# Kernel tuning notes

Hardware: AMD Instinct MI355X
Metric: run time of the kernel (lower is better)

Reference implementation:

```python
import jax, jax.numpy as jnp
import numpy as np

# dims
N, Lx, Ff = 2048, 168, 64          # batch, encoder seq len, encoder features
HID = 256                           # GRU hidden size
Ly, Ft, FOUT, BINS = 72, 22, 10, 8  # decoder steps, future feats, output size, rain classes
DEC_IN = Ft + FOUT                  # 32, GRUCell input = cat(y_t, p)
REG_H, CLS_H = 128, 128             # head hidden widths
BETA = 1.1                          # SmeLU beta


def smelu(x):
    # SmeLU: 0 for x<=-b, x for x>=b, (x+b)^2/(4b) in between
    return jnp.where(x >= BETA, x,
                     jnp.where(x <= -BETA, jnp.zeros_like(x),
                               (x + BETA) ** 2 / (4.0 * BETA)))


def gru_step(h, u, Wih, Whh, bih, bhh):
    # torch GRU/GRUCell gate math; Wih: (3H, in), Whh: (3H, H)
    gi = u @ Wih.T + bih
    gh = h @ Whh.T + bhh
    i_r, i_z, i_n = jnp.split(gi, 3, axis=-1)
    h_r, h_z, h_n = jnp.split(gh, 3, axis=-1)
    r = jax.nn.sigmoid(i_r + h_r)
    z = jax.nn.sigmoid(i_z + h_z)
    n = jnp.tanh(i_n + r * h_n)
    return (1.0 - z) * n + z * h


def setup_inputs() -> dict:
    key = jax.random.key(0)
    ks = jax.random.split(key, 24)
    s = 1.0 / np.sqrt(HID)

    def rn(k, shape, scale):
        return jax.random.normal(k, shape, dtype=jnp.float32) * scale

    return {
        'x_f': rn(ks[0], (N, Lx, Ff), 1.0),
        'x': rn(ks[1], (N, Lx, FOUT), 1.0),      # unused by forward (matches torch)
        'y_t': rn(ks[2], (N, Ly + 1, Ft), 1.0),
        'p': rn(ks[3], (N, Ly + 1, FOUT), 1.0),
        # encoder GRU (1 layer, unidirectional)
        'enc_Wih': rn(ks[4], (3 * HID, Ff), s), 'enc_Whh': rn(ks[5], (3 * HID, HID), s),
        'enc_bih': rn(ks[6], (3 * HID,), s), 'enc_bhh': rn(ks[7], (3 * HID,), s),
        # decoder GRUCell
        'dec_Wih': rn(ks[8], (3 * HID, DEC_IN), s), 'dec_Whh': rn(ks[9], (3 * HID, HID), s),
        'dec_bih': rn(ks[10], (3 * HID,), s), 'dec_bhh': rn(ks[11], (3 * HID,), s),
        # temphr head: HID -> REG_H -> (FOUT - BINS)
        'th_W0': rn(ks[12], (REG_H, HID), s), 'th_b0': rn(ks[13], (REG_H,), s),
        'th_W1': rn(ks[14], (FOUT - BINS, REG_H), 1.0 / np.sqrt(REG_H)), 'th_b1': rn(ks[15], (FOUT - BINS,), 0.05),
        # class head: HID -> CLS_H -> BINS
        'cl_W0': rn(ks[16], (CLS_H, HID), s), 'cl_b0': rn(ks[17], (CLS_H,), s),
        'cl_W1': rn(ks[18], (BINS, CLS_H), 1.0 / np.sqrt(CLS_H)), 'cl_b1': rn(ks[19], (BINS,), 0.05),
    }


def reference(x_f, x, y_t, p,
              enc_Wih, enc_Whh, enc_bih, enc_bhh,
              dec_Wih, dec_Whh, dec_bih, dec_bhh,
              th_W0, th_b0, th_W1, th_b1,
              cl_W0, cl_b0, cl_W1, cl_b1):
    # ---- encoder: run GRU over Lx, keep final hidden (N, HID) ----
    h0 = jnp.zeros((x_f.shape[0], HID), dtype=x_f.dtype)
    enc_xs = jnp.swapaxes(x_f, 0, 1)  # (Lx, N, Ff)

    def enc_body(h, u):
        return gru_step(h, u, enc_Wih, enc_Whh, enc_bih, enc_bhh), None

    h_enc, _ = jax.lax.scan(enc_body, h0, enc_xs)

    # ---- decoder inputs: torch loop uses cat(y_t,p) at index 0, then i-1 ----
    ytp = jnp.concatenate([y_t[:, :-1, :], p[:, :-1, :]], axis=-1)  # (N, Ly, DEC_IN)
    idx = jnp.concatenate([jnp.zeros((1,), jnp.int32), jnp.arange(Ly - 1, dtype=jnp.int32)])
    dec_in = jnp.swapaxes(ytp[:, idx, :], 0, 1)  # (Ly, N, DEC_IN)

    def dec_body(h, u):
        h2 = gru_step(h, u, dec_Wih, dec_Whh, dec_bih, dec_bhh)
        th = smelu(h2 @ th_W0.T + th_b0) @ th_W1.T + th_b1   # (N, 2)
        cl = smelu(h2 @ cl_W0.T + cl_b0) @ cl_W1.T + cl_b1   # (N, BINS)
        return h2, jnp.concatenate([th, cl], axis=-1)

    _, outs = jax.lax.scan(dec_body, h_enc, dec_in)  # (Ly, N, FOUT)
    return jnp.swapaxes(outs, 0, 1)  # (N, Ly, FOUT)
```

## Files before the change

### kernel.cpp

```cpp
#include <hip/hip_runtime.h>

typedef __bf16 v8bf __attribute__((ext_vector_type(8)));
typedef float v4f __attribute__((ext_vector_type(4)));
typedef float v4ff __attribute__((ext_vector_type(4)));
typedef unsigned short u16;
typedef unsigned int u32;

#define DEVI __device__ __forceinline__

constexpr int LX = 168, FF = 64;
constexpr int LY = 72, FT = 22, FOUTC = 10;
constexpr int HID = 256;
constexpr int HSTR = 264;
constexpr int UST2 = 40;
constexpr int SSTR = 264;

constexpr int W_EWIH = 0;
constexpr int W_EWHH = 49152;
constexpr int W_DWIH = 245760;
constexpr int W_DWHH = 270336;
constexpr int W_THW0 = 466944;
constexpr int W_THW1 = 499712;
constexpr int W_CLW0 = 499968;
constexpr int W_CLW1 = 532736;
constexpr int W_TOTAL = 533760;

DEVI u16 f2bf(float f) {
  u32 x; __builtin_memcpy(&x, &f, 4);
  return (u16)((x + 0x7FFFu + ((x >> 16) & 1u)) >> 16);
}
DEVI float sigm(float x) { return __builtin_amdgcn_rcpf(1.f + __expf(-x)); }
DEVI float tanh_(float x) {
  float e = __expf(-2.f * fabsf(x));
  return copysignf((1.f - e) * __builtin_amdgcn_rcpf(1.f + e), x);
}
DEVI float smelu_(float x) {
  if (x >= 1.1f) return x;
  if (x <= -1.1f) return 0.f;
  float u = x + 1.1f;
  return u * u * (1.f / 4.4f);
}
DEVI v8bf ld8(const u16* p) { return *reinterpret_cast<const v8bf*>(p); }
DEVI v4f ldw(const u16* p) { return *reinterpret_cast<const v4f*>(p); }
DEVI v8bf asbf(v4f x) { return __builtin_bit_cast(v8bf, x); }
DEVI void pin(v4f& x) { asm("" : "+v"(x)); }
DEVI v4f mfma16(v8bf a, v8bf b, v4f c) {
  return __builtin_amdgcn_mfma_f32_16x16x32_bf16(a, b, c, 0, 0, 0);
}
DEVI v8bf cvt2f(v4ff lo, v4ff hi) {
  v8bf r;
#pragma unroll
  for (int j = 0; j < 4; ++j) { r[j] = (__bf16)lo[j]; r[4 + j] = (__bf16)hi[j]; }
  return r;
}

__global__ void cvt_weights(const float* __restrict__ eWih, const float* __restrict__ eWhh,
                            const float* __restrict__ dWih, const float* __restrict__ dWhh,
                            const float* __restrict__ thW0, const float* __restrict__ thW1,
                            const float* __restrict__ clW0, const float* __restrict__ clW1,
                            u16* __restrict__ ws) {
  const int i = blockIdx.x * 256 + threadIdx.x;
  if (i >= W_TOTAL) return;
  const float* src; int off;
  if      (i < W_EWHH) { src = eWih; off = W_EWIH; }
  else if (i < W_DWIH) { src = eWhh; off = W_EWHH; }
  else if (i < W_DWHH) { src = dWih; off = W_DWIH; }
  else if (i < W_THW0) { src = dWhh; off = W_DWHH; }
  else if (i < W_THW1) { src = thW0; off = W_THW0; }
  else if (i < W_CLW0) { src = thW1; off = W_THW1; }
  else if (i < W_CLW1) { src = clW0; off = W_CLW0; }
  else                 { src = clW1; off = W_CLW1; }
  ws[i] = f2bf(src[i - off]);
}

__global__ __launch_bounds__(512, 2) void encdec_kernel(
    const float* __restrict__ xf, const float* __restrict__ yt, const float* __restrict__ pp,
    const float* __restrict__ ebih, const float* __restrict__ ebhh,
    const float* __restrict__ dbih, const float* __restrict__ dbhh,
    const float* __restrict__ thb0, const float* __restrict__ thb1,
    const float* __restrict__ clb0, const float* __restrict__ clb1,
    const u16* __restrict__ ws, float* __restrict__ outp) {
  __shared__ __align__(16) u16 slab[256 * SSTR];
  __shared__ __align__(16) u16 hls[2][16 * HSTR];
  __shared__ __align__(16) u16 a1x[16 * HSTR];
  __shared__ __align__(16) u16 uls[2][16 * UST2];

  const u16* eWih = ws + W_EWIH;
  const u16* eWhh = ws + W_EWHH;
  const u16* dWih = ws + W_DWIH;
  const u16* dWhh = ws + W_DWHH;
  const u16* thW0 = ws + W_THW0;
  const u16* thW1 = ws + W_THW1;
  const u16* clW0 = ws + W_CLW0;
  const u16* clW1 = ws + W_CLW1;

  const int tid = threadIdx.x;
  const int wave = tid >> 6;
  const int lane = tid & 63;
  const int col16 = lane & 15;
  const int quad = lane >> 4;
  const int n0 = blockIdx.x * 16;

  for (int i = tid; i < 16 * HSTR; i += 512) hls[0][i] = 0;

  float hreg[2][4];
#pragma unroll
  for (int j = 0; j < 2; ++j)
#pragma unroll
    for (int r = 0; r < 4; ++r) hreg[j][r] = 0.f;

  v4f wz[2][8], wn[2][8];
  float bsr[2], bsz[2], bin_[2], bhn[2];

  {
    for (int i = tid; i < 256 * 32; i += 512) {
      const int row = i >> 5, kb = (i & 31) << 3;
      *reinterpret_cast<v8bf*>(&slab[row * SSTR + kb]) = ld8(eWhh + row * HID + kb);
    }
#pragma unroll
    for (int j = 0; j < 2; ++j) {
      const int c = wave + 8 * j;
      const int mr = c * 16 + col16, mz = 256 + mr, mn = 512 + mr;
#pragma unroll
      for (int k = 0; k < 8; ++k) {
        wz[j][k] = ldw(eWhh + (size_t)mz * HID + k * 32 + quad * 8); pin(wz[j][k]);
        wn[j][k] = ldw(eWhh + (size_t)mn * HID + k * 32 + quad * 8); pin(wn[j][k]);
      }
      bsr[j] = ebih[mr] + ebhh[mr];
      bsz[j] = ebih[mz] + ebhh[mz];
      bin_[j] = ebih[mn];
      bhn[j] = ebhh[mn];
    }
    const float* xbase = xf + (size_t)(n0 + col16) * LX * FF + quad * 8;
    const u16* sp0 = slab + (wave * 16 + col16) * SSTR + quad * 8;
    const u16* sp1 = slab + ((wave + 8) * 16 + col16) * SSTR + quad * 8;
    __syncthreads();

#pragma unroll 1
    for (int t = 0; t < LX; ++t) {
      const float* xr = xbase + (size_t)t * FF;
      const v4ff x0 = *(const v4ff*)(xr);
      const v4ff x1 = *(const v4ff*)(xr + 4);
      const v4ff x2 = *(const v4ff*)(xr + 32);
      const v4ff x3 = *(const v4ff*)(xr + 36);
      const u16* hb = hls[t & 1] + col16 * HSTR + quad * 8;
      v8bf a[8];
#pragma unroll
      for (int k = 0; k < 8; ++k) a[k] = ld8(hb + k * 32);

      v4f az[2] = {{0.f,0.f,0.f,0.f},{0.f,0.f,0.f,0.f}};
      v4f ar[2] = {{0.f,0.f,0.f,0.f},{0.f,0.f,0.f,0.f}};
      v4f an[2] = {{0.f,0.f,0.f,0.f},{0.f,0.f,0.f,0.f}};
#pragma unroll
      for (int k = 0; k < 8; ++k) {
        az[0] = mfma16(a[k], asbf(wz[0][k]), az[0]);
        az[1] = mfma16(a[k], asbf(wz[1][k]), az[1]);
        ar[0] = mfma16(a[k], ld8(sp0 + k * 32), ar[0]);
        ar[1] = mfma16(a[k], ld8(sp1 + k * 32), ar[1]);
        an[0] = mfma16(a[k], asbf(wn[0][k]), an[0]);
        an[1] = mfma16(a[k], asbf(wn[1][k]), an[1]);
      }
      const v8bf xa0 = cvt2f(x0, x1);
      const v8bf xa1 = cvt2f(x2, x3);
      v4f ai[2] = {{0.f,0.f,0.f,0.f},{0.f,0.f,0.f,0.f}};
#pragma unroll
      for (int j = 0; j < 2; ++j) {
        const int m = (wave + 8 * j) * 16 + col16;
        const u16* pwr = eWih + (size_t)m * FF + quad * 8;
        const u16* pwz = eWih + (size_t)(256 + m) * FF + quad * 8;
        const u16* pwn = eWih + (size_t)(512 + m) * FF + quad * 8;
        az[j] = mfma16(xa0, ld8(pwz), az[j]);
        az[j] = mfma16(xa1, ld8(pwz + 32), az[j]);
        ar[j] = mfma16(xa0, ld8(pwr), ar[j]);
        ar[j] = mfma16(xa1, ld8(pwr + 32), ar[j]);
        ai[j] = mfma16(xa0, ld8(pwn), ai[j]);
        ai[j] = mfma16(xa1, ld8(pwn + 32), ai[j]);
      }
#pragma unroll
      for (int j = 0; j < 2; ++j) {
        const int cidx = (wave + 8 * j) * 16 + col16;
#pragma unroll
        for (int r = 0; r < 4; ++r) {
          const float zg = sigm(az[j][r] + bsz[j]);
          const float rg = sigm(ar[j][r] + bsr[j]);
          const float ng = tanh_(ai[j][r] + bin_[j] + rg * (an[j][r] + bhn[j]));
          hreg[j][r] = (1.f - zg) * ng + zg * hreg[j][r];
          hls[(t + 1) & 1][(quad * 4 + r) * HSTR + cidx] = f2bf(hreg[j][r]);
        }
      }
      __syncthreads();
    }
  }

  {
    for (int i = tid; i < 256 * 32; i += 512) {
      const int row = i >> 5, kb = (i & 31) << 3;
      *reinterpret_cast<v8bf*>(&slab[row * SSTR + kb]) = ld8(dWhh + row * HID + kb);
    }
    float hb0[2];
#pragma unroll
    for (int j = 0; j < 2; ++j) {
      const int c = wave + 8 * j;
      const int mr = c * 16 + col16, mz = 256 + mr, mn = 512 + mr;
#pragma unroll
      for (int k = 0; k < 8; ++k) {
        wz[j][k] = ldw(dWhh + (size_t)mz * HID + k * 32 + quad * 8); pin(wz[j][k]);
        wn[j][k] = ldw(dWhh + (size_t)mn * HID + k * 32 + quad * 8); pin(wn[j][k]);
      }
      bsr[j] = dbih[mr] + dbhh[mr];
      bsz[j] = dbih[mz] + dbhh[mz];
      bin_[j] = dbih[mn];
      bhn[j] = dbhh[mn];
      const int ml = wave * 16 + col16;
      hb0[j] = (j == 0) ? thb0[ml] : clb0[ml];
    }
    const bool w1th = (col16 < 2);
    const bool w1cl = (col16 >= 2 && col16 < FOUTC);
    const float b1v = w1th ? thb1[col16] : (w1cl ? clb1[col16 - 2] : 0.f);
    const u16* sp0 = slab + (wave * 16 + col16) * SSTR + quad * 8;
    const u16* sp1 = slab + ((wave + 8) * 16 + col16) * SSTR + quad * 8;

    const int srr = tid >> 5, scc = tid & 31;
    const size_t ybase = (size_t)(n0 + srr) * (LY + 1);
    {
      const float v = (scc < FT) ? yt[ybase * FT + scc] : pp[ybase * FOUTC + (scc - FT)];
      uls[0][srr * UST2 + scc] = f2bf(v);
    }
    __syncthreads();

#pragma unroll 1
    for (int t = 0; t < LY; ++t) {
      float un = 0.f;
      if (t + 1 < LY)
        un = (scc < FT) ? yt[(ybase + t) * FT + scc]
                        : pp[(ybase + t) * FOUTC + (scc - FT)];
      const v8bf ua = ld8(uls[t & 1] + col16 * UST2 + quad * 8);
      const u16* hb = hls[0] + col16 * HSTR + quad * 8;
      v8bf a[8];
#pragma unroll
      for (int k = 0; k < 8; ++k) a[k] = ld8(hb + k * 32);
      __syncthreads();

      if (wave == 0 && t >= 2) {
        const u16* arow = ((t & 1) ? a1x : hls[1]) + col16 * HSTR + quad * 8;
        v4f acc = {0.f, 0.f, 0.f, 0.f};
#pragma unroll
        for (int kt = 0; kt < 8; ++kt) {
          v8bf b;
#pragma unroll
          for (int j = 0; j < 8; ++j) b[j] = (__bf16)0.0f;
          if (kt < 4) { if (w1th) b = ld8(thW1 + col16 * 128 + kt * 32 + quad * 8); }
          else        { if (w1cl) b = ld8(clW1 + (col16 - 2) * 128 + (kt - 4) * 32 + quad * 8); }
          acc = mfma16(ld8(arow + kt * 32), b, acc);
        }
        if (col16 < FOUTC) {
#pragma unroll
          for (int r = 0; r < 4; ++r)
            outp[((size_t)(n0 + quad * 4 + r) * LY + (t - 2)) * FOUTC + col16] =
                acc[r] + b1v;
        }
      }

      v4f az[2] = {{0.f,0.f,0.f,0.f},{0.f,0.f,0.f,0.f}};
      v4f ar[2] = {{0.f,0.f,0.f,0.f},{0.f,0.f,0.f,0.f}};
      v4f an[2] = {{0.f,0.f,0.f,0.f},{0.f,0.f,0.f,0.f}};
#pragma unroll
      for (int k = 0; k < 8; ++k) {
        az[0] = mfma16(a[k], asbf(wz[0][k]), az[0]);
        az[1] = mfma16(a[k], asbf(wz[1][k]), az[1]);
        ar[0] = mfma16(a[k], ld8(sp0 + k * 32), ar[0]);
        ar[1] = mfma16(a[k], ld8(sp1 + k * 32), ar[1]);
        an[0] = mfma16(a[k], asbf(wn[0][k]), an[0]);
        an[1] = mfma16(a[k], asbf(wn[1][k]), an[1]);
      }
      v4f ai[2] = {{0.f,0.f,0.f,0.f},{0.f,0.f,0.f,0.f}};
#pragma unroll
      for (int j = 0; j < 2; ++j) {
        const int m = (wave + 8 * j) * 16 + col16;
        az[j] = mfma16(ua, ld8(dWih + (size_t)(256 + m) * 32 + quad * 8), az[j]);
        ar[j] = mfma16(ua, ld8(dWih + (size_t)m * 32 + quad * 8), ar[j]);
        ai[j] = mfma16(ua, ld8(dWih + (size_t)(512 + m) * 32 + quad * 8), ai[j]);
      }
#pragma unroll
      for (int j = 0; j < 2; ++j) {
        const int cidx = (wave + 8 * j) * 16 + col16;
#pragma unroll
        for (int r = 0; r < 4; ++r) {
          const float zg = sigm(az[j][r] + bsz[j]);
          const float rg = sigm(ar[j][r] + bsr[j]);
          const float ng = tanh_(ai[j][r] + bin_[j] + rg * (an[j][r] + bhn[j]));
          hreg[j][r] = (1.f - zg) * ng + zg * hreg[j][r];
          hls[0][(quad * 4 + r) * HSTR + cidx] = f2bf(hreg[j][r]);
        }
      }

      if (t >= 1) {
        u16* a1w = ((t - 1) & 1) ? a1x : hls[1];
#pragma unroll
        for (int j = 0; j < 2; ++j) {
          const u16* W0 = (j == 0) ? thW0 : clW0;
          const u16* pw = W0 + (size_t)(wave * 16 + col16) * HID + quad * 8;
          v4f acc = {0.f, 0.f, 0.f, 0.f};
#pragma unroll
          for (int k = 0; k < 8; ++k) acc = mfma16(a[k], ld8(pw + k * 32), acc);
          const int c = wave + 8 * j;
#pragma unroll
          for (int r = 0; r < 4; ++r)
            a1w[(quad * 4 + r) * HSTR + c * 16 + col16] =
                f2bf(smelu_(acc[r] + hb0[j]));
        }
      }
      if (t + 1 < LY) uls[(t + 1) & 1][srr * UST2 + scc] = f2bf(un);
      __syncthreads();
    }

    {
      const u16* h2b = hls[0] + col16 * HSTR + quad * 8;
      v8bf ah2[8];
#pragma unroll
      for (int k = 0; k < 8; ++k) ah2[k] = ld8(h2b + k * 32);
      u16* a1w = ((LY - 1) & 1) ? a1x : hls[1];
#pragma unroll
      for (int j = 0; j < 2; ++j) {
        const u16* W0 = (j == 0) ? thW0 : clW0;
        const u16* pw = W0 + (size_t)(wave * 16 + col16) * HID + quad * 8;
        v4f acc = {0.f, 0.f, 0.f, 0.f};
#pragma unroll
        for (int k = 0; k < 8; ++k) acc = mfma16(ah2[k], ld8(pw + k * 32), acc);
        const int c = wave + 8 * j;
#pragma unroll
        for (int r = 0; r < 4; ++r)
          a1w[(quad * 4 + r) * HSTR + c * 16 + col16] =
              f2bf(smelu_(acc[r] + hb0[j]));
      }
      if (wave == 0) {
        const u16* arow = (((LY - 2) & 1) ? a1x : hls[1]) + col16 * HSTR + quad * 8;
        v4f acc = {0.f, 0.f, 0.f, 0.f};
#pragma unroll
        for (int kt = 0; kt < 8; ++kt) {
          v8bf b;
#pragma unroll
          for (int j = 0; j < 8; ++j) b[j] = (__bf16)0.0f;
          if (kt < 4) { if (w1th) b = ld8(thW1 + col16 * 128 + kt * 32 + quad * 8); }
          else        { if (w1cl) b = ld8(clW1 + (col16 - 2) * 128 + (kt - 4) * 32 + quad * 8); }
          acc = mfma16(ld8(arow + kt * 32), b, acc);
        }
        if (col16 < FOUTC) {
#pragma unroll
          for (int r = 0; r < 4; ++r)
            outp[((size_t)(n0 + quad * 4 + r) * LY + (LY - 2)) * FOUTC + col16] =
                acc[r] + b1v;
        }
      }
      __syncthreads();
      if (wave == 0) {
        const u16* arow = (((LY - 1) & 1) ? a1x : hls[1]) + col16 * HSTR + quad * 8;
        v4f acc = {0.f, 0.f, 0.f, 0.f};
#pragma unroll
        for (int kt = 0; kt < 8; ++kt) {
          v8bf b;
#pragma unroll
          for (int j = 0; j < 8; ++j) b[j] = (__bf16)0.0f;
          if (kt < 4) { if (w1th) b = ld8(thW1 + col16 * 128 + kt * 32 + quad * 8); }
          else        { if (w1cl) b = ld8(clW1 + (col16 - 2) * 128 + (kt - 4) * 32 + quad * 8); }
          acc = mfma16(ld8(arow + kt * 32), b, acc);
        }
        if (col16 < FOUTC) {
#pragma unroll
          for (int r = 0; r < 4; ++r)
            outp[((size_t)(n0 + quad * 4 + r) * LY + (LY - 1)) * FOUTC + col16] =
                acc[r] + b1v;
        }
      }
    }
  }
}

extern "C" void kernel_launch(void* const* d_in, const int* in_sizes, int n_in,
                              void* d_out, int out_size, void* d_ws, size_t ws_size,
                              hipStream_t stream) {
  (void)in_sizes; (void)n_in; (void)ws_size; (void)out_size;
  const float* xf   = (const float*)d_in[0];
  const float* yt   = (const float*)d_in[2];
  const float* pp   = (const float*)d_in[3];
  const float* eWih = (const float*)d_in[4];
  const float* eWhh = (const float*)d_in[5];
  const float* ebih = (const float*)d_in[6];
  const float* ebhh = (const float*)d_in[7];
  const float* dWih = (const float*)d_in[8];
  const float* dWhh = (const float*)d_in[9];
  const float* dbih = (const float*)d_in[10];
  const float* dbhh = (const float*)d_in[11];
  const float* thW0 = (const float*)d_in[12];
  const float* thb0 = (const float*)d_in[13];
  const float* thW1 = (const float*)d_in[14];
  const float* thb1 = (const float*)d_in[15];
  const float* clW0 = (const float*)d_in[16];
  const float* clb0 = (const float*)d_in[17];
  const float* clW1 = (const float*)d_in[18];
  const float* clb1 = (const float*)d_in[19];
  float* outp = (float*)d_out;
  u16* ws = (u16*)d_ws;

  cvt_weights<<<dim3((W_TOTAL + 255) / 256), dim3(256), 0, stream>>>(
      eWih, eWhh, dWih, dWhh, thW0, thW1, clW0, clW1, ws);
  encdec_kernel<<<dim3(128), dim3(512), 0, stream>>>(
      xf, yt, pp, ebih, ebhh, dbih, dbhh, thb0, thb1, clb0, clb1, ws, outp);
}
```

Baseline: 1.180 ms.

## Double block to 16 waves, one hidden column tile per wave, stage x via LDS

The recurrent kernel now runs 1024 threads per block, so each wave owns a single 16-column slice of the hidden state instead of two. This halves the serial MFMA chain and the register-resident weights per wave. Encoder inputs are prefetched one step ahead into a double-buffered LDS tile, each wave converting one row to bf16, rather than every lane loading fp32 x directly. Biases are folded into the accumulator initial values, and the decoder head now splits the first-layer GEMM across waves (th vs cl) and uses a ping-pong hidden buffer with an extra barrier per step. The risks are higher register pressure under the 1024-thread launch bound and more barrier cost per timestep.

```diff
diff --git a/kernel.cpp b/kernel.cpp
--- a/kernel.cpp
+++ b/kernel.cpp
@@ -2,7 +2,6 @@
 
 typedef __bf16 v8bf __attribute__((ext_vector_type(8)));
 typedef float v4f __attribute__((ext_vector_type(4)));
-typedef float v4ff __attribute__((ext_vector_type(4)));
 typedef unsigned short u16;
 typedef unsigned int u32;
 
@@ -14,6 +13,7 @@
 constexpr int HSTR = 264;
 constexpr int UST2 = 40;
 constexpr int SSTR = 264;
+constexpr int XSTR = 72;
 
 constexpr int W_EWIH = 0;
 constexpr int W_EWHH = 49152;
@@ -46,12 +46,6 @@
 DEVI void pin(v4f& x) { asm("" : "+v"(x)); }
 DEVI v4f mfma16(v8bf a, v8bf b, v4f c) {
   return __builtin_amdgcn_mfma_f32_16x16x32_bf16(a, b, c, 0, 0, 0);
-}
-DEVI v8bf cvt2f(v4ff lo, v4ff hi) {
-  v8bf r;
-#pragma unroll
-  for (int j = 0; j < 4; ++j) { r[j] = (__bf16)lo[j]; r[4 + j] = (__bf16)hi[j]; }
-  return r;
 }
 
 __global__ void cvt_weights(const float* __restrict__ eWih, const float* __restrict__ eWhh,
@@ -73,7 +67,7 @@
   ws[i] = f2bf(src[i - off]);
 }
 
-__global__ __launch_bounds__(512, 2) void encdec_kernel(
+__global__ __launch_bounds__(1024, 4) void encdec_kernel(
     const float* __restrict__ xf, const float* __restrict__ yt, const float* __restrict__ pp,
     const float* __restrict__ ebih, const float* __restrict__ ebhh,
     const float* __restrict__ dbih, const float* __restrict__ dbhh,
@@ -82,7 +76,7 @@
     const u16* __restrict__ ws, float* __restrict__ outp) {
   __shared__ __align__(16) u16 slab[256 * SSTR];
   __shared__ __align__(16) u16 hls[2][16 * HSTR];
-  __shared__ __align__(16) u16 a1x[16 * HSTR];
+  __shared__ __align__(16) u16 aux[16 * HSTR];
   __shared__ __align__(16) u16 uls[2][16 * UST2];
 
   const u16* eWih = ws + W_EWIH;
@@ -101,278 +95,193 @@
   const int quad = lane >> 4;
   const int n0 = blockIdx.x * 16;
 
-  for (int i = tid; i < 16 * HSTR; i += 512) hls[0][i] = 0;
-
-  float hreg[2][4];
-#pragma unroll
-  for (int j = 0; j < 2; ++j)
-#pragma unroll
-    for (int r = 0; r < 4; ++r) hreg[j][r] = 0.f;
-
-  v4f wz[2][8], wn[2][8];
-  float bsr[2], bsz[2], bin_[2], bhn[2];
+  const int cidx = wave * 16 + col16;
+  const int mr = cidx, mz = 256 + cidx, mn = 512 + cidx;
+
+  float hreg[4] = {0.f, 0.f, 0.f, 0.f};
+
+  v4f wz[8], wn[8];
+  float bsr, bsz, bin_, bhn;
+
+  const int xk = lane;
+  const float* xsrc = xf + ((size_t)(n0 + wave) * LX) * FF + xk;
 
   {
-    for (int i = tid; i < 256 * 32; i += 512) {
+    for (int i = tid; i < 256 * 32; i += 1024) {
       const int row = i >> 5, kb = (i & 31) << 3;
       *reinterpret_cast<v8bf*>(&slab[row * SSTR + kb]) = ld8(eWhh + row * HID + kb);
     }
-#pragma unroll
-    for (int j = 0; j < 2; ++j) {
-      const int c = wave + 8 * j;
-      const int mr = c * 16 + col16, mz = 256 + mr, mn = 512 + mr;
-#pragma unroll
-      for (int k = 0; k < 8; ++k) {
-        wz[j][k] = ldw(eWhh + (size_t)mz * HID + k * 32 + quad * 8); pin(wz[j][k]);
-        wn[j][k] = ldw(eWhh + (size_t)mn * HID + k * 32 + quad * 8); pin(wn[j][k]);
-      }
-      bsr[j] = ebih[mr] + ebhh[mr];
-      bsz[j] = ebih[mz] + ebhh[mz];
-      bin_[j] = ebih[mn];
-      bhn[j] = ebhh[mn];
-    }
-    const float* xbase = xf + (size_t)(n0 + col16) * LX * FF + quad * 8;
-    const u16* sp0 = slab + (wave * 16 + col16) * SSTR + quad * 8;
-    const u16* sp1 = slab + ((wave + 8) * 16 + col16) * SSTR + quad * 8;
+    for (int i = tid; i < 16 * HSTR; i += 1024) hls[0][i] = 0;
+    aux[wave * XSTR + xk] = f2bf(xsrc[0]);
+#pragma unroll
+    for (int k = 0; k < 8; ++k) {
+      wz[k] = ldw(eWhh + (size_t)mz * HID + k * 32 + quad * 8); pin(wz[k]);
+      wn[k] = ldw(eWhh + (size_t)mn * HID + k * 32 + quad * 8); pin(wn[k]);
+    }
+    bsr = ebih[mr] + ebhh[mr];
+    bsz = ebih[mz] + ebhh[mz];
+    bin_ = ebih[mn];
+    bhn = ebhh[mn];
+
+    const u16* sp  = slab + cidx * SSTR + quad * 8;
+    const u16* pwr = eWih + (size_t)mr * FF + quad * 8;
+    const u16* pwz = eWih + (size_t)mz * FF + quad * 8;
+    const u16* pwn = eWih + (size_t)mn * FF + quad * 8;
     __syncthreads();
 
 #pragma unroll 1
     for (int t = 0; t < LX; ++t) {
-      const float* xr = xbase + (size_t)t * FF;
-      const v4ff x0 = *(const v4ff*)(xr);
-      const v4ff x1 = *(const v4ff*)(xr + 4);
-      const v4ff x2 = *(const v4ff*)(xr + 32);
-      const v4ff x3 = *(const v4ff*)(xr + 36);
+      float xnext = 0.f;
+      if (t + 1 < LX) xnext = xsrc[(size_t)(t + 1) * FF];
+
       const u16* hb = hls[t & 1] + col16 * HSTR + quad * 8;
-      v8bf a[8];
-#pragma unroll
-      for (int k = 0; k < 8; ++k) a[k] = ld8(hb + k * 32);
-
-      v4f az[2] = {{0.f,0.f,0.f,0.f},{0.f,0.f,0.f,0.f}};
-      v4f ar[2] = {{0.f,0.f,0.f,0.f},{0.f,0.f,0.f,0.f}};
-      v4f an[2] = {{0.f,0.f,0.f,0.f},{0.f,0.f,0.f,0.f}};
+      v4f az = {bsz, bsz, bsz, bsz};
+      v4f ar = {bsr, bsr, bsr, bsr};
+      v4f an = {bhn, bhn, bhn, bhn};
+      v4f ai = {bin_, bin_, bin_, bin_};
 #pragma unroll
       for (int k = 0; k < 8; ++k) {
-        az[0] = mfma16(a[k], asbf(wz[0][k]), az[0]);
-        az[1] = mfma16(a[k], asbf(wz[1][k]), az[1]);
-        ar[0] = mfma16(a[k], ld8(sp0 + k * 32), ar[0]);
-        ar[1] = mfma16(a[k], ld8(sp1 + k * 32), ar[1]);
-        an[0] = mfma16(a[k], asbf(wn[0][k]), an[0]);
-        an[1] = mfma16(a[k], asbf(wn[1][k]), an[1]);
-      }
-      const v8bf xa0 = cvt2f(x0, x1);
-      const v8bf xa1 = cvt2f(x2, x3);
-      v4f ai[2] = {{0.f,0.f,0.f,0.f},{0.f,0.f,0.f,0.f}};
-#pragma unroll
-      for (int j = 0; j < 2; ++j) {
-        const int m = (wave + 8 * j) * 16 + col16;
-        const u16* pwr = eWih + (size_t)m * FF + quad * 8;
-        const u16* pwz = eWih + (size_t)(256 + m) * FF + quad * 8;
-        const u16* pwn = eWih + (size_t)(512 + m) * FF + quad * 8;
-        az[j] = mfma16(xa0, ld8(pwz), az[j]);
-        az[j] = mfma16(xa1, ld8(pwz + 32), az[j]);
-        ar[j] = mfma16(xa0, ld8(pwr), ar[j]);
-        ar[j] = mfma16(xa1, ld8(pwr + 32), ar[j]);
-        ai[j] = mfma16(xa0, ld8(pwn), ai[j]);
-        ai[j] = mfma16(xa1, ld8(pwn + 32), ai[j]);
-      }
-#pragma unroll
-      for (int j = 0; j < 2; ++j) {
-        const int cidx = (wave + 8 * j) * 16 + col16;
-#pragma unroll
-        for (int r = 0; r < 4; ++r) {
-          const float zg = sigm(az[j][r] + bsz[j]);
-          const float rg = sigm(ar[j][r] + bsr[j]);
-          const float ng = tanh_(ai[j][r] + bin_[j] + rg * (an[j][r] + bhn[j]));
-          hreg[j][r] = (1.f - zg) * ng + zg * hreg[j][r];
-          hls[(t + 1) & 1][(quad * 4 + r) * HSTR + cidx] = f2bf(hreg[j][r]);
-        }
-      }
+        const v8bf a = ld8(hb + k * 32);
+        az = mfma16(a, asbf(wz[k]), az);
+        ar = mfma16(a, ld8(sp + k * 32), ar);
+        an = mfma16(a, asbf(wn[k]), an);
+      }
+      const u16* xb = aux + (t & 1) * (16 * XSTR) + col16 * XSTR + quad * 8;
+      const v8bf xa0 = ld8(xb);
+      const v8bf xa1 = ld8(xb + 32);
+      az = mfma16(xa0, ld8(pwz), az);
+      az = mfma16(xa1, ld8(pwz + 32), az);
+      ar = mfma16(xa0, ld8(pwr), ar);
+      ar = mfma16(xa1, ld8(pwr + 32), ar);
+      ai = mfma16(xa0, ld8(pwn), ai);
+      ai = mfma16(xa1, ld8(pwn + 32), ai);
+#pragma unroll
+      for (int r = 0; r < 4; ++r) {
+        const float zg = sigm(az[r]);
+        const float rg = sigm(ar[r]);
+        const float ng = tanh_(ai[r] + rg * an[r]);
+        hreg[r] = (1.f - zg) * ng + zg * hreg[r];
+        hls[(t + 1) & 1][(quad * 4 + r) * HSTR + cidx] = f2bf(hreg[r]);
+      }
+      if (t + 1 < LX)
+        aux[((t + 1) & 1) * (16 * XSTR) + wave * XSTR + xk] = f2bf(xnext);
       __syncthreads();
     }
   }
 
   {
-    for (int i = tid; i < 256 * 32; i += 512) {
+    for (int i = tid; i < 256 * 32; i += 1024) {
       const int row = i >> 5, kb = (i & 31) << 3;
       *reinterpret_cast<v8bf*>(&slab[row * SSTR + kb]) = ld8(dWhh + row * HID + kb);
     }
-    float hb0[2];
-#pragma unroll
-    for (int j = 0; j < 2; ++j) {
-      const int c = wave + 8 * j;
-      const int mr = c * 16 + col16, mz = 256 + mr, mn = 512 + mr;
-#pragma unroll
-      for (int k = 0; k < 8; ++k) {
-        wz[j][k] = ldw(dWhh + (size_t)mz * HID + k * 32 + quad * 8); pin(wz[j][k]);
-        wn[j][k] = ldw(dWhh + (size_t)mn * HID + k * 32 + quad * 8); pin(wn[j][k]);
-      }
-      bsr[j] = dbih[mr] + dbhh[mr];
-      bsz[j] = dbih[mz] + dbhh[mz];
-      bin_[j] = dbih[mn];
-      bhn[j] = dbhh[mn];
-      const int ml = wave * 16 + col16;
-      hb0[j] = (j == 0) ? thb0[ml] : clb0[ml];
-    }
+#pragma unroll
+    for (int k = 0; k < 8; ++k) {
+      wz[k] = ldw(dWhh + (size_t)mz * HID + k * 32 + quad * 8); pin(wz[k]);
+      wn[k] = ldw(dWhh + (size_t)mn * HID + k * 32 + quad * 8); pin(wn[k]);
+    }
+    bsr = dbih[mr] + dbhh[mr];
+    bsz = dbih[mz] + dbhh[mz];
+    bin_ = dbih[mn];
+    bhn = dbhh[mn];
+
+    const bool isTh = (wave < 8);
+    const int wrow = (wave & 7) * 16 + col16;
+    const u16* pW0 = (isTh ? thW0 : clW0) + (size_t)wrow * HID + quad * 8;
+    const float hb0 = isTh ? thb0[wrow] : clb0[wrow];
+
     const bool w1th = (col16 < 2);
     const bool w1cl = (col16 >= 2 && col16 < FOUTC);
     const float b1v = w1th ? thb1[col16] : (w1cl ? clb1[col16 - 2] : 0.f);
-    const u16* sp0 = slab + (wave * 16 + col16) * SSTR + quad * 8;
-    const u16* sp1 = slab + ((wave + 8) * 16 + col16) * SSTR + quad * 8;
+
+    const u16* sp  = slab + cidx * SSTR + quad * 8;
+    const u16* pur = dWih + (size_t)mr * 32 + quad * 8;
+    const u16* puz = dWih + (size_t)mz * 32 + quad * 8;
+    const u16* pun = dWih + (size_t)mn * 32 + quad * 8;
 
     const int srr = tid >> 5, scc = tid & 31;
     const size_t ybase = (size_t)(n0 + srr) * (LY + 1);
-    {
+    if (tid < 512) {
       const float v = (scc < FT) ? yt[ybase * FT + scc] : pp[ybase * FOUTC + (scc - FT)];
       uls[0][srr * UST2 + scc] = f2bf(v);
     }
+
+    auto gemm2 = [&](int s) {
+      const u16* arow = aux + col16 * HSTR + quad * 8;
+      v4f acc = {0.f, 0.f, 0.f, 0.f};
+#pragma unroll
+      for (int kt = 0; kt < 8; ++kt) {
+        v8bf b;
+#pragma unroll
+        for (int j = 0; j < 8; ++j) b[j] = (__bf16)0.0f;
+        if (kt < 4) { if (w1th) b = ld8(thW1 + col16 * 128 + kt * 32 + quad * 8); }
+        else        { if (w1cl) b = ld8(clW1 + (col16 - 2) * 128 + (kt - 4) * 32 + quad * 8); }
+        acc = mfma16(ld8(arow + kt * 32), b, acc);
+      }
+      if (col16 < FOUTC) {
+#pragma unroll
+        for (int r = 0; r < 4; ++r)
+          outp[((size_t)(n0 + quad * 4 + r) * LY + s) * FOUTC + col16] = acc[r] + b1v;
+      }
+    };
+
+    auto gemm1 = [&](const u16* hbase) {
+      const u16* hA = hbase + col16 * HSTR + quad * 8;
+      v4f acc = {0.f, 0.f, 0.f, 0.f};
+#pragma unroll
+      for (int k = 0; k < 8; ++k)
+        acc = mfma16(ld8(hA + k * 32), ld8(pW0 + k * 32), acc);
+#pragma unroll
+      for (int r = 0; r < 4; ++r)
+        aux[(quad * 4 + r) * HSTR + cidx] = f2bf(smelu_(acc[r] + hb0));
+    };
+
     __syncthreads();
 
 #pragma unroll 1
     for (int t = 0; t < LY; ++t) {
       float un = 0.f;
-      if (t + 1 < LY)
+      if (tid < 512 && t + 1 < LY)
         un = (scc < FT) ? yt[(ybase + t) * FT + scc]
                         : pp[(ybase + t) * FOUTC + (scc - FT)];
+
+      if (wave == 0 && t >= 2) gemm2(t - 2);
+
       const v8bf ua = ld8(uls[t & 1] + col16 * UST2 + quad * 8);
-      const u16* hb = hls[0] + col16 * HSTR + quad * 8;
-      v8bf a[8];
-#pragma unroll
-      for (int k = 0; k < 8; ++k) a[k] = ld8(hb + k * 32);
+      const u16* hb = hls[t & 1] + col16 * HSTR + quad * 8;
+      v4f az = {bsz, bsz, bsz, bsz};
+      v4f ar = {bsr, bsr, bsr, bsr};
+      v4f an = {bhn, bhn, bhn, bhn};
+      v4f ai = {bin_, bin_, bin_, bin_};
+#pragma unroll
+      for (int k = 0; k < 8; ++k) {
+        const v8bf a = ld8(hb + k * 32);
+        az = mfma16(a, asbf(wz[k]), az);
+        ar = mfma16(a, ld8(sp + k * 32), ar);
+        an = mfma16(a, asbf(wn[k]), an);
+      }
+      az = mfma16(ua, ld8(puz), az);
+      ar = mfma16(ua, ld8(pur), ar);
+      ai = mfma16(ua, ld8(pun), ai);
+#pragma unroll
+      for (int r = 0; r < 4; ++r) {
+        const float zg = sigm(az[r]);
+        const float rg = sigm(ar[r]);
+        const float ng = tanh_(ai[r] + rg * an[r]);
+        hreg[r] = (1.f - zg) * ng + zg * hreg[r];
+        hls[(t + 1) & 1][(quad * 4 + r) * HSTR + cidx] = f2bf(hreg[r]);
+      }
+      if (tid < 512 && t + 1 < LY) uls[(t + 1) & 1][srr * UST2 + scc] = f2bf(un);
       __syncthreads();
 
-      if (wave == 0 && t >= 2) {
-        const u16* arow = ((t & 1) ? a1x : hls[1]) + col16 * HSTR + quad * 8;
-        v4f acc = {0.f, 0.f, 0.f, 0.f};
-#pragma unroll
-        for (int kt = 0; kt < 8; ++kt) {
-          v8bf b;
-#pragma unroll
-          for (int j = 0; j < 8; ++j) b[j] = (__bf16)0.0f;
-          if (kt < 4) { if (w1th) b = ld8(thW1 + col16 * 128 + kt * 32 + quad * 8); }
-          else        { if (w1cl) b = ld8(clW1 + (col16 - 2) * 128 + (kt - 4) * 32 + quad * 8); }
-          acc = mfma16(ld8(arow + kt * 32), b, acc);
-        }
-        if (col16 < FOUTC) {
-#pragma unroll
-          for (int r = 0; r < 4; ++r)
-            outp[((size_t)(n0 + quad * 4 + r) * LY + (t - 2)) * FOUTC + col16] =
-                acc[r] + b1v;
-        }
-      }
-
-      v4f az[2] = {{0.f,0.f,0.f,0.f},{0.f,0.f,0.f,0.f}};
-      v4f ar[2] = {{0.f,0.f,0.f,0.f},{0.f,0.f,0.f,0.f}};
-      v4f an[2] = {{0.f,0.f,0.f,0.f},{0.f,0.f,0.f,0.f}};
-#pragma unroll
-      for (int k = 0; k < 8; ++k) {
-        az[0] = mfma16(a[k], asbf(wz[0][k]), az[0]);
-        az[1] = mfma16(a[k], asbf(wz[1][k]), az[1]);
-        ar[0] = mfma16(a[k], ld8(sp0 + k * 32), ar[0]);
-        ar[1] = mfma16(a[k], ld8(sp1 + k * 32), ar[1]);
-        an[0] = mfma16(a[k], asbf(wn[0][k]), an[0]);
-        an[1] = mfma16(a[k], asbf(wn[1][k]), an[1]);
-      }
-      v4f ai[2] = {{0.f,0.f,0.f,0.f},{0.f,0.f,0.f,0.f}};
-#pragma unroll
-      for (int j = 0; j < 2; ++j) {
-        const int m = (wave + 8 * j) * 16 + col16;
-        az[j] = mfma16(ua, ld8(dWih + (size_t)(256 + m) * 32 + quad * 8), az[j]);
-        ar[j] = mfma16(ua, ld8(dWih + (size_t)m * 32 + quad * 8), ar[j]);
-        ai[j] = mfma16(ua, ld8(dWih + (size_t)(512 + m) * 32 + quad * 8), ai[j]);
-      }
-#pragma unroll
-      for (int j = 0; j < 2; ++j) {
-        const int cidx = (wave + 8 * j) * 16 + col16;
-#pragma unroll
-        for (int r = 0; r < 4; ++r) {
-          const float zg = sigm(az[j][r] + bsz[j]);
-          const float rg = sigm(ar[j][r] + bsr[j]);
-          const float ng = tanh_(ai[j][r] + bin_[j] + rg * (an[j][r] + bhn[j]));
-          hreg[j][r] = (1.f - zg) * ng + zg * hreg[j][r];
-          hls[0][(quad * 4 + r) * HSTR + cidx] = f2bf(hreg[j][r]);
-        }
-      }
-
-      if (t >= 1) {
-        u16* a1w = ((t - 1) & 1) ? a1x : hls[1];
-#pragma unroll
-        for (int j = 0; j < 2; ++j) {
-          const u16* W0 = (j == 0) ? thW0 : clW0;
-          const u16* pw = W0 + (size_t)(wave * 16 + col16) * HID + quad * 8;
-          v4f acc = {0.f, 0.f, 0.f, 0.f};
-#pragma unroll
-          for (int k = 0; k < 8; ++k) acc = mfma16(a[k], ld8(pw + k * 32), acc);
-          const int c = wave + 8 * j;
-#pragma unroll
-          for (int r = 0; r < 4; ++r)
-            a1w[(quad * 4 + r) * HSTR + c * 16 + col16] =
-                f2bf(smelu_(acc[r] + hb0[j]));
-        }
-      }
-      if (t + 1 < LY) uls[(t + 1) & 1][srr * UST2 + scc] = f2bf(un);
+      if (t >= 1) gemm1(hls[t & 1]);
       __syncthreads();
     }
 
-    {
-      const u16* h2b = hls[0] + col16 * HSTR + quad * 8;
-      v8bf ah2[8];
-#pragma unroll
-      for (int k = 0; k < 8; ++k) ah2[k] = ld8(h2b + k * 32);
-      u16* a1w = ((LY - 1) & 1) ? a1x : hls[1];
-#pragma unroll
-      for (int j = 0; j < 2; ++j) {
-        const u16* W0 = (j == 0) ? thW0 : clW0;
-        const u16* pw = W0 + (size_t)(wave * 16 + col16) * HID + quad * 8;
-        v4f acc = {0.f, 0.f, 0.f, 0.f};
-#pragma unroll
-        for (int k = 0; k < 8; ++k) acc = mfma16(ah2[k], ld8(pw + k * 32), acc);
-        const int c = wave + 8 * j;
-#pragma unroll
-        for (int r = 0; r < 4; ++r)
-          a1w[(quad * 4 + r) * HSTR + c * 16 + col16] =
-              f2bf(smelu_(acc[r] + hb0[j]));
-      }
-      if (wave == 0) {
-        const u16* arow = (((LY - 2) & 1) ? a1x : hls[1]) + col16 * HSTR + quad * 8;
-        v4f acc = {0.f, 0.f, 0.f, 0.f};
-#pragma unroll
-        for (int kt = 0; kt < 8; ++kt) {
-          v8bf b;
-#pragma unroll
-          for (int j = 0; j < 8; ++j) b[j] = (__bf16)0.0f;
-          if (kt < 4) { if (w1th) b = ld8(thW1 + col16 * 128 + kt * 32 + quad * 8); }
-          else        { if (w1cl) b = ld8(clW1 + (col16 - 2) * 128 + (kt - 4) * 32 + quad * 8); }
-          acc = mfma16(ld8(arow + kt * 32), b, acc);
-        }
-        if (col16 < FOUTC) {
-#pragma unroll
-          for (int r = 0; r < 4; ++r)
-            outp[((size_t)(n0 + quad * 4 + r) * LY + (LY - 2)) * FOUTC + col16] =
-                acc[r] + b1v;
-        }
-      }
-      __syncthreads();
-      if (wave == 0) {
-        const u16* arow = (((LY - 1) & 1) ? a1x : hls[1]) + col16 * HSTR + quad * 8;
-        v4f acc = {0.f, 0.f, 0.f, 0.f};
-#pragma unroll
-        for (int kt = 0; kt < 8; ++kt) {
-          v8bf b;
-#pragma unroll
-          for (int j = 0; j < 8; ++j) b[j] = (__bf16)0.0f;
-          if (kt < 4) { if (w1th) b = ld8(thW1 + col16 * 128 + kt * 32 + quad * 8); }
-          else        { if (w1cl) b = ld8(clW1 + (col16 - 2) * 128 + (kt - 4) * 32 + quad * 8); }
-          acc = mfma16(ld8(arow + kt * 32), b, acc);
-        }
-        if (col16 < FOUTC) {
-#pragma unroll
-          for (int r = 0; r < 4; ++r)
-            outp[((size_t)(n0 + quad * 4 + r) * LY + (LY - 1)) * FOUTC + col16] =
-                acc[r] + b1v;
-        }
-      }
-    }
+    if (wave == 0) gemm2(LY - 2);
+    __syncthreads();
+    gemm1(hls[LY & 1]);
+    __syncthreads();
+    if (wave == 0) gemm2(LY - 1);
   }
 }
 
@@ -404,6 +313,6 @@
 
   cvt_weights<<<dim3((W_TOTAL + 255) / 256), dim3(256), 0, stream>>>(
       eWih, eWhh, dWih, dWhh, thW0, thW1, clW0, clW1, ws);
-  encdec_kernel<<<dim3(128), dim3(512), 0, stream>>>(
+  encdec_kernel<<<dim3(128), dim3(1024), 0, stream>>>(
       xf, yt, pp, ebih, ebhh, dbih, dbhh, thb0, thb1, clb0, clb1, ws, outp);
 }
```

Measured after the change: 1.364 ms. 1.16x slower.
